# Optimization experiments

Hardware: AMD Instinct MI355X
Metric: run time of the kernel (lower is better)

Reference implementation:

```python
import jax, jax.numpy as jnp
import numpy as np

THETA = 10000.0

def _rope_cache(seq_len, d_k, dtype=jnp.float32):
    # theta_k = theta ** (-(2i/d_k)), angles[n, i] = n * theta_k[i]
    inv_freq = THETA ** (-(jnp.arange(0, d_k, 2, dtype=jnp.float32) / d_k))
    pos = jnp.arange(seq_len, dtype=jnp.float32)
    ang = pos[:, None] * inv_freq[None, :]          # [S, d_k/2]
    cos = jnp.repeat(jnp.cos(ang), 2, axis=-1)      # [S, d_k]
    sin = jnp.repeat(jnp.sin(ang), 2, axis=-1)
    return cos.astype(dtype), sin.astype(dtype)

def _apply_rope(x, cos, sin):
    # x: [..., S, d_k]; rotate even/odd pairs: rot[2i] = -x[2i+1], rot[2i+1] = x[2i]
    x2 = x.reshape(x.shape[:-1] + (x.shape[-1] // 2, 2))
    rot = jnp.stack([-x2[..., 1], x2[..., 0]], axis=-1).reshape(x.shape)
    return x * cos + rot * sin

def setup_inputs() -> dict:
    key = jax.random.key(0)
    ks = jax.random.split(key, 5)
    B, S, D = 2, 2048, 1024
    H, DK = 16, 64
    scale = (2.0 / (D + DK)) ** 0.5
    x = jax.random.normal(ks[0], (B, S, D), dtype=jnp.float32)
    Wq = jax.random.normal(ks[1], (H, D, DK), dtype=jnp.float32) * scale
    Wk = jax.random.normal(ks[2], (H, D, DK), dtype=jnp.float32) * scale
    Wv = jax.random.normal(ks[3], (H, D, DK), dtype=jnp.float32) * scale
    Wo = jax.random.normal(ks[4], (D, D), dtype=jnp.float32) * (2.0 / (2 * D)) ** 0.5
    return {"x": x, "Wq": Wq, "Wk": Wk, "Wv": Wv, "Wo": Wo}

def reference(x, Wq, Wk, Wv, Wo):
    B, S, D = x.shape
    H, _, DK = Wq.shape
    cos, sin = _rope_cache(S, DK, x.dtype)          # [S, DK]
    q = jnp.einsum('bsd,hdk->bhsk', x, Wq)
    k = jnp.einsum('bsd,hdk->bhsk', x, Wk)
    v = jnp.einsum('bsd,hdk->bhsk', x, Wv)
    q = _apply_rope(q, cos, sin)
    k = _apply_rope(k, cos, sin)
    scores = jnp.einsum('bhqk,bhsk->bhqs', q, k) / jnp.sqrt(jnp.asarray(DK, x.dtype))
    causal = jnp.tril(jnp.ones((S, S), dtype=bool))
    scores = jnp.where(causal, scores, -jnp.inf)
    attn = jax.nn.softmax(scores, axis=-1)
    out = jnp.einsum('bhqs,bhsk->bhqk', attn, v)    # [B,H,S,DK]
    out = out.transpose(0, 2, 1, 3).reshape(B, S, H * DK)  # concat heads
    return jnp.einsum('bsd,do->bso', out, Wo)
```

## Files before the change

### kernel.cpp

```cpp
#include <hip/hip_runtime.h>
#include <math.h>

typedef __attribute__((ext_vector_type(8))) short bf16x8;
typedef __attribute__((ext_vector_type(4))) float f32x4;
typedef __attribute__((ext_vector_type(16))) float f32x16;
typedef __attribute__((ext_vector_type(4))) unsigned int uint32x4;
typedef __attribute__((ext_vector_type(2))) unsigned int uint32x2;
typedef unsigned short ushort_t;
typedef unsigned int uint_t;

typedef const void __attribute__((address_space(1)))* gas_ptr;
typedef void __attribute__((address_space(3)))* las_ptr;

namespace {

constexpr int S_  = 2048;
constexpr int D_  = 1024;
constexpr float CSC = 0.18033688011f;

__device__ inline ushort_t f2bf(float f) {
    uint_t u = __builtin_bit_cast(uint_t, f);
    u += 0x7FFFu + ((u >> 16) & 1u);
    return (ushort_t)(u >> 16);
}
__device__ inline uint_t cvtpk(float lo, float hi) {
    uint_t r;
    asm("v_cvt_pk_bf16_f32 %0, %1, %2" : "=v"(r) : "v"(lo), "v"(hi));
    return r;
}
__device__ inline void plswap(uint_t& d, uint_t& s) {
    uint32x2 r = __builtin_amdgcn_permlane32_swap(d, s, false, false);
    d = r[0];
    s = r[1];
}
__device__ inline float xhalf_sum(float x) {
    uint_t d = __builtin_bit_cast(uint_t, x), s = d;
    plswap(d, s);
    return __builtin_bit_cast(float, d) + __builtin_bit_cast(float, s);
}

__device__ inline void tconv_body(const float* __restrict__ src,
                                  ushort_t* __restrict__ dst,
                                  int R, int C, int r0, int c0, int tid)
{
    __shared__ float Tl[64][65];
    #pragma unroll
    for (int l = 0; l < 4; ++l) {
        int i = tid + l * 256;
        int row = i >> 4, col = (i & 15) * 4;
        float4 v = *(const float4*)(src + (size_t)(r0 + row) * C + c0 + col);
        Tl[row][col] = v.x; Tl[row][col + 1] = v.y;
        Tl[row][col + 2] = v.z; Tl[row][col + 3] = v.w;
    }
    __syncthreads();
    #pragma unroll
    for (int l = 0; l < 4; ++l) {
        int i = tid + l * 256;
        int cc = i >> 4, rr = (i & 15) * 4;
        uint_t lo = (uint_t)f2bf(Tl[rr][cc])     | ((uint_t)f2bf(Tl[rr + 1][cc]) << 16);
        uint_t hi = (uint_t)f2bf(Tl[rr + 2][cc]) | ((uint_t)f2bf(Tl[rr + 3][cc]) << 16);
        *(uint2*)(dst + (size_t)(c0 + cc) * R + r0 + rr) = make_uint2(lo, hi);
    }
}

__global__ __launch_bounds__(256)
void prep_kernel(const float* __restrict__ x,  const float* __restrict__ Wq,
                 const float* __restrict__ Wk, const float* __restrict__ Wv,
                 const float* __restrict__ Wo,
                 ushort_t* __restrict__ xb, ushort_t* __restrict__ Wt,
                 ushort_t* __restrict__ Wot, float* __restrict__ tbl)
{
    const int b = blockIdx.x, tid = threadIdx.x;
    if (b < 2048) {
        int i = b * 256 + tid;
        float4 a = ((const float4*)x)[i * 2];
        float4 c = ((const float4*)x)[i * 2 + 1];
        uint_t u0 = (uint_t)f2bf(a.x) | ((uint_t)f2bf(a.y) << 16);
        uint_t u1 = (uint_t)f2bf(a.z) | ((uint_t)f2bf(a.w) << 16);
        uint_t u2 = (uint_t)f2bf(c.x) | ((uint_t)f2bf(c.y) << 16);
        uint_t u3 = (uint_t)f2bf(c.z) | ((uint_t)f2bf(c.w) << 16);
        ((uint4*)xb)[i] = make_uint4(u0, u1, u2, u3);
    } else if (b < 2304) {
        int i = (b - 2048) * 256 + tid;
        int s = i >> 5, p = i & 31;
        float inv = powf(10000.0f, -(float)p * (1.0f / 32.0f));
        float sn, cs;
        sincosf((float)s * inv, &sn, &cs);
        ((float2*)tbl)[i] = make_float2(cs, sn);
    } else if (b < 3072) {
        int lin = b - 2304;
        int z = lin >> 4, rx = lin & 15;
        const float* src = (z < 16 ? Wq : z < 32 ? Wk : Wv) + (size_t)(z & 15) * 65536;
        tconv_body(src, Wt + (size_t)z * 65536, 1024, 64, rx * 64, 0, tid);
    } else {
        int lin = b - 3072;
        tconv_body(Wo, Wot, 1024, 1024, (lin & 15) * 64, (lin >> 4) * 64, tid);
    }
}

__global__ __launch_bounds__(256)
void gemm_kernel(const ushort_t* __restrict__ A, const ushort_t* __restrict__ Bt,
                 ushort_t* __restrict__ Qo, ushort_t* __restrict__ Ko,
                 ushort_t* __restrict__ Vto,
                 const float* __restrict__ tbl, int K)
{
    __shared__ char smem[49152];

    const int tid  = threadIdx.x;
    const int w    = tid >> 6, lane = tid & 63;
    const int lq   = lane & 15, lk = lane >> 4;
    const int wr   = w >> 1, wc = w & 1;
    const int m0   = blockIdx.x * 128;
    const int n0   = blockIdx.y * 128;

    f32x4 acc[4][4] = {};

    const int c0s  = tid, c1s = 256 + tid;
    const int row0 = c0s >> 2, cc0 = (c0s & 3) * 8;
    const int row1 = c1s >> 2, cc1 = (c1s & 3) * 8;
    const ushort_t* gA0 = A  + (size_t)(m0 + row0) * K + cc0;
    const ushort_t* gA1 = A  + (size_t)(m0 + row1) * K + cc1;
    const ushort_t* gB0 = Bt + (size_t)(n0 + row0) * K + cc0;
    const ushort_t* gB1 = Bt + (size_t)(n0 + row1) * K + cc1;
    const int lds0 = c0s * 16;
    const int lds1 = c1s * 16;

    auto stage = [&](int buf, int k0) {
        char* As = smem + buf * 16384;
        char* Bs = As + 8192;
        __builtin_amdgcn_global_load_lds((gas_ptr)(gA0 + k0), (las_ptr)(As + lds0), 16, 0, 0);
        __builtin_amdgcn_global_load_lds((gas_ptr)(gA1 + k0), (las_ptr)(As + lds1), 16, 0, 0);
        __builtin_amdgcn_global_load_lds((gas_ptr)(gB0 + k0), (las_ptr)(Bs + lds0), 16, 0, 0);
        __builtin_amdgcn_global_load_lds((gas_ptr)(gB1 + k0), (las_ptr)(Bs + lds1), 16, 0, 0);
    };

    stage(0, 0);

    const int NT = K >> 5;
    int cur = 0, nx = 1;
    for (int t = 0; t < NT; ++t) {
        if (t < NT - 1) {
            stage(nx, (t + 1) << 5);
            asm volatile("s_waitcnt vmcnt(4)" ::: "memory");
        } else {
            asm volatile("s_waitcnt vmcnt(0)" ::: "memory");
        }
        __builtin_amdgcn_s_barrier();
        asm volatile("" ::: "memory");

        const char* As = smem + cur * 16384;
        const char* Bs = As + 8192;
        bf16x8 a[4], b[4];
        #pragma unroll
        for (int m = 0; m < 4; ++m)
            a[m] = *(const bf16x8*)(As + (wr * 64 + m * 16 + lq) * 64 + lk * 16);
        #pragma unroll
        for (int n = 0; n < 4; ++n)
            b[n] = *(const bf16x8*)(Bs + (wc * 64 + n * 16 + lq) * 64 + lk * 16);
        #pragma unroll
        for (int m = 0; m < 4; ++m)
            #pragma unroll
            for (int n = 0; n < 4; ++n)
                acc[m][n] = __builtin_amdgcn_mfma_f32_16x16x32_bf16(a[m], b[n], acc[m][n], 0, 0, 0);

        asm volatile("" ::: "memory");

        cur = (cur == 2) ? 0 : cur + 1;
        nx  = (nx  == 2) ? 0 : nx  + 1;
    }

    __syncthreads();

    const int sel = n0 >> 10;
    ushort_t* EP = (ushort_t*)smem;
    const int h0 = (n0 & 1023) >> 6;
    if (sel < 2) {
        const float sc = (sel == 0) ? CSC : 1.0f;
        #pragma unroll
        for (int m = 0; m < 4; ++m) {
            #pragma unroll
            for (int r = 0; r < 4; ++r) {
                int lrow = wr * 64 + m * 16 + lk * 4 + r;
                int sG = (m0 + lrow) & 2047;
                #pragma unroll
                for (int n = 0; n < 4; ++n) {
                    int lcol = wc * 64 + n * 16 + lq;
                    int dk = lcol & 63;
                    float v = acc[m][n][r] * sc;
                    float2 cs = *(const float2*)(tbl + ((size_t)sG * 32 + (dk >> 1)) * 2);
                    float sp = __shfl_xor(v, 1);
                    float rv = (dk & 1) ? (v * cs.x + sp * cs.y)
                                        : (v * cs.x - sp * cs.y);
                    EP[lrow * 136 + lcol] = f2bf(rv);
                }
            }
        }
        __syncthreads();
        ushort_t* dst = (sel == 0) ? Qo : Ko;
        #pragma unroll
        for (int it = 0; it < 8; ++it) {
            int idx = it * 256 + tid;
            int row = idx >> 4, c16 = idx & 15;
            uint4 v = *(const uint4*)(EP + row * 136 + c16 * 8);
            int mg = m0 + row;
            int b_ = mg >> 11, s = mg & 2047;
            int h = h0 + (c16 >> 3);
            int dk0 = (c16 & 7) * 8;
            *(uint4*)(dst + (((size_t)b_ * 16 + h) * 2048 + s) * 64 + dk0) = v;
        }
    } else {
        #pragma unroll
        for (int m = 0; m < 4; ++m) {
            #pragma unroll
            for (int r = 0; r < 4; ++r) {
                int lrow = wr * 64 + m * 16 + lk * 4 + r;
                #pragma unroll
                for (int n = 0; n < 4; ++n) {
                    int lcol = wc * 64 + n * 16 + lq;
                    EP[lcol * 136 + lrow] = f2bf(acc[m][n][r]);
                }
            }
        }
        __syncthreads();
        #pragma unroll
        for (int it = 0; it < 8; ++it) {
            int idx = it * 256 + tid;
            int col = idx >> 4, c16 = idx & 15;
            uint4 v = *(const uint4*)(EP + col * 136 + c16 * 8);
            int h = h0 + (col >> 6);
            int dk = col & 63;
            int sb = m0 + c16 * 8;
            int b_ = sb >> 11, s = sb & 2047;
            *(uint4*)(Vto + (((size_t)b_ * 16 + h) * 64 + dk) * 2048 + s) = v;
        }
    }
}

__global__ __launch_bounds__(256)
void gemm2_kernel(const ushort_t* __restrict__ A, const ushort_t* __restrict__ Bt,
                  float* __restrict__ Co, int K)
{
    __shared__ char smem[36864];

    const int tid = threadIdx.x;
    const int w = tid >> 6, lane = tid & 63;
    const int lq = lane & 15, lk = lane >> 4;
    const int wr = w >> 1, wc = w & 1;
    const int m0 = blockIdx.x * 64;
    const int n0 = blockIdx.y * 128;

    f32x4 acc[2][4] = {};

    const int rowA = tid >> 2, cA = (tid & 3) * 8;
    const ushort_t* gA = A + (size_t)(m0 + rowA) * K + cA;
    const int sB0 = tid, sB1 = 256 + tid;
    const int rB0 = sB0 >> 2, cB0 = (sB0 & 3) * 8;
    const int rB1 = sB1 >> 2, cB1 = (sB1 & 3) * 8;
    const ushort_t* gB0 = Bt + (size_t)(n0 + rB0) * K + cB0;
    const ushort_t* gB1 = Bt + (size_t)(n0 + rB1) * K + cB1;

    auto stage = [&](int buf, int k0) {
        char* base = smem + buf * 12288;
        __builtin_amdgcn_global_load_lds((gas_ptr)(gA + k0),  (las_ptr)(base + tid * 16), 16, 0, 0);
        __builtin_amdgcn_global_load_lds((gas_ptr)(gB0 + k0), (las_ptr)(base + 4096 + sB0 * 16), 16, 0, 0);
        __builtin_amdgcn_global_load_lds((gas_ptr)(gB1 + k0), (las_ptr)(base + 4096 + sB1 * 16), 16, 0, 0);
    };

    stage(0, 0);

    const int NT = K >> 5;
    int cur = 0, nx = 1;
    for (int t = 0; t < NT; ++t) {
        if (t < NT - 1) {
            stage(nx, (t + 1) << 5);
            asm volatile("s_waitcnt vmcnt(3)" ::: "memory");
        } else {
            asm volatile("s_waitcnt vmcnt(0)" ::: "memory");
        }
        __builtin_amdgcn_s_barrier();
        asm volatile("" ::: "memory");

        const char* As = smem + cur * 12288;
        const char* Bs = As + 4096;
        bf16x8 a[2], b[4];
        #pragma unroll
        for (int m = 0; m < 2; ++m)
            a[m] = *(const bf16x8*)(As + (wr * 32 + m * 16 + lq) * 64 + lk * 16);
        #pragma unroll
        for (int n = 0; n < 4; ++n)
            b[n] = *(const bf16x8*)(Bs + (wc * 64 + n * 16 + lq) * 64 + lk * 16);
        #pragma unroll
        for (int m = 0; m < 2; ++m)
            #pragma unroll
            for (int n = 0; n < 4; ++n)
                acc[m][n] = __builtin_amdgcn_mfma_f32_16x16x32_bf16(a[m], b[n], acc[m][n], 0, 0, 0);

        asm volatile("" ::: "memory");

        cur = (cur == 2) ? 0 : cur + 1;
        nx  = (nx  == 2) ? 0 : nx  + 1;
    }

    float* EPf = (float*)smem;
    #pragma unroll
    for (int c = 0; c < 2; ++c) {
        __syncthreads();
        if (wr == c) {
            #pragma unroll
            for (int m = 0; m < 2; ++m)
                #pragma unroll
                for (int r = 0; r < 4; ++r) {
                    int lrow = m * 16 + lk * 4 + r;
                    #pragma unroll
                    for (int n = 0; n < 4; ++n) {
                        int lcol = wc * 64 + n * 16 + lq;
                        EPf[lrow * 132 + lcol] = acc[m][n][r];
                    }
                }
        }
        __syncthreads();
        #pragma unroll
        for (int it = 0; it < 4; ++it) {
            int idx = it * 256 + tid;
            int rl = idx >> 5, c32 = idx & 31;
            float4 v = *(const float4*)(EPf + rl * 132 + c32 * 4);
            *(float4*)(Co + (size_t)(m0 + c * 32 + rl) * D_ + n0 + c32 * 4) = v;
        }
    }
}

__global__ __launch_bounds__(512)
void attn_kernel(const ushort_t* __restrict__ Q, const ushort_t* __restrict__ Kg,
                 const ushort_t* __restrict__ Vt, ushort_t* __restrict__ O)
{
    __shared__ ushort_t Ks[2][128 * 64];
    __shared__ ushort_t Vs[2][64 * 128];

    const int bid = blockIdx.x;
    const int p  = 31 - (bid >> 5);
    const int bh = bid & 31;

    const int tid = threadIdx.x;
    const int w = tid >> 6, lane = tid & 63;
    const int wq = w & 1, st = w >> 1;
    const int lq = lane & 31, hi = lane >> 5;
    const size_t bhBase = (size_t)bh * S_ * 64;

    const int nt   = (p >> 1) + 1;
    const int qrel = ((p & 1) << 1) + wq;

    bf16x8 qf[4];
    {
        const ushort_t* qp = Q + bhBase + (size_t)(p * 64 + wq * 32 + lq) * 64 + hi * 8;
        qf[0] = *(const bf16x8*)(qp);
        qf[1] = *(const bf16x8*)(qp + 16);
        qf[2] = *(const bf16x8*)(qp + 32);
        qf[3] = *(const bf16x8*)(qp + 48);
    }

    const int slot0 = tid, slot1 = 512 + tid;
    const int rK0 = slot0 >> 3, rK1 = slot1 >> 3;
    const int rV0 = slot0 >> 4, rV1 = slot1 >> 4;
    const ushort_t* gk0 = Kg + bhBase + (size_t)rK0 * 64 + ((slot0 & 7) ^ (rK0 & 7)) * 8;
    const ushort_t* gk1 = Kg + bhBase + (size_t)rK1 * 64 + ((slot1 & 7) ^ (rK1 & 7)) * 8;
    const ushort_t* gv0 = Vt + bhBase + (size_t)rV0 * 2048 + ((slot0 & 15) ^ (rV0 & 7)) * 8;
    const ushort_t* gv1 = Vt + bhBase + (size_t)rV1 * 2048 + ((slot1 & 15) ^ (rV1 & 7)) * 8;

    auto stage = [&](int buf, int t) {
        const size_t ko = (size_t)t * 128 * 64;
        const size_t vo = (size_t)t * 128;
        __builtin_amdgcn_global_load_lds((gas_ptr)(gk0 + ko), (las_ptr)((char*)Ks[buf] + slot0 * 16), 16, 0, 0);
        __builtin_amdgcn_global_load_lds((gas_ptr)(gk1 + ko), (las_ptr)((char*)Ks[buf] + slot1 * 16), 16, 0, 0);
        __builtin_amdgcn_global_load_lds((gas_ptr)(gv0 + vo), (las_ptr)((char*)Vs[buf] + slot0 * 16), 16, 0, 0);
        __builtin_amdgcn_global_load_lds((gas_ptr)(gv1 + vo), (las_ptr)((char*)Vs[buf] + slot1 * 16), 16, 0, 0);
    };

    float l = 0.0f;
    f32x16 oacc[2] = {};

    const int krow = st * 32 + lq;

    stage(0, 0);

    for (int t = 0; t < nt; ++t) {
        const int cur = t & 1;
        if (t < nt - 1) {
            stage(cur ^ 1, t + 1);
            asm volatile("s_waitcnt vmcnt(4)" ::: "memory");
        } else {
            asm volatile("s_waitcnt vmcnt(0)" ::: "memory");
        }
        __builtin_amdgcn_s_barrier();
        asm volatile("" ::: "memory");

        const bool last = (t == nt - 1);
        if (!(last && st > qrel)) {
            f32x16 sacc = {};
            #pragma unroll
            for (int c = 0; c < 4; ++c) {
                int koff = krow * 128 + ((c * 32 + hi * 16) ^ ((krow & 7) << 4));
                bf16x8 kf = *(const bf16x8*)((const char*)Ks[cur] + koff);
                sacc = __builtin_amdgcn_mfma_f32_32x32x16_bf16(kf, qf[c], sacc, 0, 0, 0);
            }

            if (last && st == qrel) {
                #pragma unroll
                for (int idx = 0; idx < 16; ++idx) {
                    int kvl = (idx & 3) + 8 * (idx >> 2) + 4 * hi;
                    if (kvl > lq) sacc[idx] = -1e30f;
                }
            }

            float pv[16];
            #pragma unroll
            for (int idx = 0; idx < 16; ++idx) {
                float v = exp2f(sacc[idx] - 32.0f);
                pv[idx] = v;
                l += v;
            }

            #pragma unroll
            for (int c2 = 0; c2 < 2; ++c2) {
                uint_t w0 = cvtpk(pv[8 * c2 + 0], pv[8 * c2 + 1]);
                uint_t w1 = cvtpk(pv[8 * c2 + 2], pv[8 * c2 + 3]);
                uint_t w2 = cvtpk(pv[8 * c2 + 4], pv[8 * c2 + 5]);
                uint_t w3 = cvtpk(pv[8 * c2 + 6], pv[8 * c2 + 7]);
                plswap(w0, w2);
                plswap(w1, w3);
                uint32x4 pw; pw[0] = w0; pw[1] = w1; pw[2] = w2; pw[3] = w3;
                bf16x8 pb = __builtin_bit_cast(bf16x8, pw);
                #pragma unroll
                for (int d2 = 0; d2 < 2; ++d2) {
                    int vrow = d2 * 32 + lq;
                    int vslot = (st * 4 + c2 * 2 + hi) ^ (vrow & 7);
                    bf16x8 vf = *(const bf16x8*)((const char*)Vs[cur] + vrow * 256 + vslot * 16);
                    oacc[d2] = __builtin_amdgcn_mfma_f32_32x32x16_bf16(vf, pb, oacc[d2], 0, 0, 0);
                }
            }
        }
        asm volatile("" ::: "memory");
        __builtin_amdgcn_s_barrier();
        asm volatile("" ::: "memory");
    }

    l = xhalf_sum(l);

    __syncthreads();

    float* ksf = (float*)Ks;
    float* vsf = (float*)Vs;
    const int rowi = wq * 64 + lane;
    vsf[st * 128 + rowi] = l;
    if (st == 3) {
        #pragma unroll
        for (int j = 0; j < 8; ++j) {
            f32x4 v4;
            v4[0] = oacc[j >> 2][(j & 3) * 4 + 0];
            v4[1] = oacc[j >> 2][(j & 3) * 4 + 1];
            v4[2] = oacc[j >> 2][(j & 3) * 4 + 2];
            v4[3] = oacc[j >> 2][(j & 3) * 4 + 3];
            *(f32x4*)(ksf + rowi * 32 + ((j ^ (rowi & 7)) * 4)) = v4;
        }
    }
    __syncthreads();
    if (st == 2) {
        #pragma unroll
        for (int j = 0; j < 8; ++j) {
            int soff = rowi * 32 + ((j ^ (rowi & 7)) * 4);
            f32x4 v4 = *(const f32x4*)(ksf + soff);
            v4[0] += oacc[j >> 2][(j & 3) * 4 + 0];
            v4[1] += oacc[j >> 2][(j & 3) * 4 + 1];
            v4[2] += oacc[j >> 2][(j & 3) * 4 + 2];
            v4[3] += oacc[j >> 2][(j & 3) * 4 + 3];
            *(f32x4*)(ksf + soff) = v4;
        }
    }
    __syncthreads();
    if (st == 1) {
        #pragma unroll
        for (int j = 0; j < 8; ++j) {
            int soff = rowi * 32 + ((j ^ (rowi & 7)) * 4);
            f32x4 v4 = *(const f32x4*)(ksf + soff);
            v4[0] += oacc[j >> 2][(j & 3) * 4 + 0];
            v4[1] += oacc[j >> 2][(j & 3) * 4 + 1];
            v4[2] += oacc[j >> 2][(j & 3) * 4 + 2];
            v4[3] += oacc[j >> 2][(j & 3) * 4 + 3];
            *(f32x4*)(ksf + soff) = v4;
        }
    }
    __syncthreads();
    if (st == 0) {
        float lt = vsf[rowi] + vsf[128 + rowi] + vsf[256 + rowi] + vsf[384 + rowi];
        float inv = 1.0f / lt;
        const int b_ = bh >> 4, h = bh & 15;
        const int s = p * 64 + wq * 32 + lq;
        ushort_t* ob = O + ((size_t)b_ * 2048 + s) * 1024 + h * 64;
        #pragma unroll
        for (int j = 0; j < 8; ++j) {
            int soff = rowi * 32 + ((j ^ (rowi & 7)) * 4);
            f32x4 v4 = *(const f32x4*)(ksf + soff);
            int d2 = j >> 2, base = (j & 3) * 4;
            float q0 = (oacc[d2][base + 0] + v4[0]) * inv;
            float q1 = (oacc[d2][base + 1] + v4[1]) * inv;
            float q2 = (oacc[d2][base + 2] + v4[2]) * inv;
            float q3 = (oacc[d2][base + 3] + v4[3]) * inv;
            uint2 pkv;
            pkv.x = cvtpk(q0, q1);
            pkv.y = cvtpk(q2, q3);
            *(uint2*)(ob + d2 * 32 + 8 * (j & 3) + 4 * hi) = pkv;
        }
    }
}

}

extern "C" void kernel_launch(void* const* d_in, const int* in_sizes, int n_in,
                              void* d_out, int out_size, void* d_ws, size_t ws_size,
                              hipStream_t stream)
{
    const float* x  = (const float*)d_in[0];
    const float* Wq = (const float*)d_in[1];
    const float* Wk = (const float*)d_in[2];
    const float* Wv = (const float*)d_in[3];
    const float* Wo = (const float*)d_in[4];

    ushort_t* xb  = (ushort_t*)d_ws;
    ushort_t* Wt  = xb  + 4194304;
    ushort_t* Wot = Wt  + 3145728;
    ushort_t* Qb  = Wot + 1048576;
    ushort_t* Kb  = Qb  + 4194304;
    ushort_t* Vtb = Kb  + 4194304;
    ushort_t* Ob  = Vtb + 4194304;
    float*    tbl = (float*)(Ob + 4194304);

    prep_kernel<<<3328, 256, 0, stream>>>(x, Wq, Wk, Wv, Wo, xb, Wt, Wot, tbl);

    gemm_kernel<<<dim3(32, 24), 256, 0, stream>>>(xb, Wt, Qb, Kb, Vtb, tbl, 1024);

    attn_kernel<<<1024, 512, 0, stream>>>(Qb, Kb, Vtb, Ob);

    gemm2_kernel<<<dim3(64, 8), 256, 0, stream>>>(Ob, Wot, (float*)d_out, 1024);
}
```

Baseline: 103.7 us.

## Widen attention query tile to 128 rows per block with two key splits

Each attention block now covers 128 query rows: four query warps times two key-split groups, instead of 64 rows with four key splits. Each staged K/V tile is therefore reused by twice as many queries, halving global K/V traffic and the block count. The cross-warp reduction at the end shrinks from a four-way to a two-way combine. Block order is changed to mix long and short causal rows. In exchange each warp handles two 32-key chunks per tile, and there are fewer blocks to balance the causal work across CUs.

```diff
diff --git a/kernel.cpp b/kernel.cpp
--- a/kernel.cpp
+++ b/kernel.cpp
@@ -337,21 +337,23 @@
     __shared__ ushort_t Vs[2][64 * 128];
 
     const int bid = blockIdx.x;
-    const int p  = 31 - (bid >> 5);
-    const int bh = bid & 31;
+    const int cch = bid >> 8;
+    const int jj  = bid & 255;
+    const int pg  = jj >> 5;
+    const int bh  = jj & 31;
+    const int P   = cch ? pg : 15 - pg;
 
     const int tid = threadIdx.x;
     const int w = tid >> 6, lane = tid & 63;
-    const int wq = w & 1, st = w >> 1;
+    const int wq = w & 3, st = w >> 2;
     const int lq = lane & 31, hi = lane >> 5;
     const size_t bhBase = (size_t)bh * S_ * 64;
 
-    const int nt   = (p >> 1) + 1;
-    const int qrel = ((p & 1) << 1) + wq;
+    const int nt = P + 1;
 
     bf16x8 qf[4];
     {
-        const ushort_t* qp = Q + bhBase + (size_t)(p * 64 + wq * 32 + lq) * 64 + hi * 8;
+        const ushort_t* qp = Q + bhBase + (size_t)(P * 128 + wq * 32 + lq) * 64 + hi * 8;
         qf[0] = *(const bf16x8*)(qp);
         qf[1] = *(const bf16x8*)(qp + 16);
         qf[2] = *(const bf16x8*)(qp + 32);
@@ -378,8 +380,6 @@
     float l = 0.0f;
     f32x16 oacc[2] = {};
 
-    const int krow = st * 32 + lq;
-
     stage(0, 0);
 
     for (int t = 0; t < nt; ++t) {
@@ -394,16 +394,25 @@
         asm volatile("" ::: "memory");
 
         const bool last = (t == nt - 1);
-        if (!(last && st > qrel)) {
+        #pragma unroll
+        for (int ch = 0; ch < 2; ++ch) {
+            bool tri = false;
+            if (last) {
+                int kb = st * 2 + ch;
+                if (kb > wq) continue;
+                tri = (kb == wq);
+            }
+
+            const int krow = st * 64 + ch * 32 + lq;
             f32x16 sacc = {};
             #pragma unroll
-            for (int c = 0; c < 4; ++c) {
-                int koff = krow * 128 + ((c * 32 + hi * 16) ^ ((krow & 7) << 4));
+            for (int cc = 0; cc < 4; ++cc) {
+                int koff = krow * 128 + ((cc * 32 + hi * 16) ^ ((krow & 7) << 4));
                 bf16x8 kf = *(const bf16x8*)((const char*)Ks[cur] + koff);
-                sacc = __builtin_amdgcn_mfma_f32_32x32x16_bf16(kf, qf[c], sacc, 0, 0, 0);
-            }
-
-            if (last && st == qrel) {
+                sacc = __builtin_amdgcn_mfma_f32_32x32x16_bf16(kf, qf[cc], sacc, 0, 0, 0);
+            }
+
+            if (tri) {
                 #pragma unroll
                 for (int idx = 0; idx < 16; ++idx) {
                     int kvl = (idx & 3) + 8 * (idx >> 2) + 4 * hi;
@@ -432,7 +441,7 @@
                 #pragma unroll
                 for (int d2 = 0; d2 < 2; ++d2) {
                     int vrow = d2 * 32 + lq;
-                    int vslot = (st * 4 + c2 * 2 + hi) ^ (vrow & 7);
+                    int vslot = (st * 8 + ch * 4 + c2 * 2 + hi) ^ (vrow & 7);
                     bf16x8 vf = *(const bf16x8*)((const char*)Vs[cur] + vrow * 256 + vslot * 16);
                     oacc[d2] = __builtin_amdgcn_mfma_f32_32x32x16_bf16(vf, pb, oacc[d2], 0, 0, 0);
                 }
@@ -450,56 +459,30 @@
     float* ksf = (float*)Ks;
     float* vsf = (float*)Vs;
     const int rowi = wq * 64 + lane;
-    vsf[st * 128 + rowi] = l;
-    if (st == 3) {
-        #pragma unroll
-        for (int j = 0; j < 8; ++j) {
+    vsf[st * 256 + rowi] = l;
+    if (st == 1) {
+        #pragma unroll
+        for (int j2 = 0; j2 < 8; ++j2) {
             f32x4 v4;
-            v4[0] = oacc[j >> 2][(j & 3) * 4 + 0];
-            v4[1] = oacc[j >> 2][(j & 3) * 4 + 1];
-            v4[2] = oacc[j >> 2][(j & 3) * 4 + 2];
-            v4[3] = oacc[j >> 2][(j & 3) * 4 + 3];
-            *(f32x4*)(ksf + rowi * 32 + ((j ^ (rowi & 7)) * 4)) = v4;
-        }
-    }
-    __syncthreads();
-    if (st == 2) {
-        #pragma unroll
-        for (int j = 0; j < 8; ++j) {
-            int soff = rowi * 32 + ((j ^ (rowi & 7)) * 4);
-            f32x4 v4 = *(const f32x4*)(ksf + soff);
-            v4[0] += oacc[j >> 2][(j & 3) * 4 + 0];
-            v4[1] += oacc[j >> 2][(j & 3) * 4 + 1];
-            v4[2] += oacc[j >> 2][(j & 3) * 4 + 2];
-            v4[3] += oacc[j >> 2][(j & 3) * 4 + 3];
-            *(f32x4*)(ksf + soff) = v4;
-        }
-    }
-    __syncthreads();
-    if (st == 1) {
-        #pragma unroll
-        for (int j = 0; j < 8; ++j) {
-            int soff = rowi * 32 + ((j ^ (rowi & 7)) * 4);
-            f32x4 v4 = *(const f32x4*)(ksf + soff);
-            v4[0] += oacc[j >> 2][(j & 3) * 4 + 0];
-            v4[1] += oacc[j >> 2][(j & 3) * 4 + 1];
-            v4[2] += oacc[j >> 2][(j & 3) * 4 + 2];
-            v4[3] += oacc[j >> 2][(j & 3) * 4 + 3];
-            *(f32x4*)(ksf + soff) = v4;
+            v4[0] = oacc[j2 >> 2][(j2 & 3) * 4 + 0];
+            v4[1] = oacc[j2 >> 2][(j2 & 3) * 4 + 1];
+            v4[2] = oacc[j2 >> 2][(j2 & 3) * 4 + 2];
+            v4[3] = oacc[j2 >> 2][(j2 & 3) * 4 + 3];
+            *(f32x4*)(ksf + rowi * 32 + ((j2 ^ (rowi & 7)) * 4)) = v4;
         }
     }
     __syncthreads();
     if (st == 0) {
-        float lt = vsf[rowi] + vsf[128 + rowi] + vsf[256 + rowi] + vsf[384 + rowi];
+        float lt = vsf[rowi] + vsf[256 + rowi];
         float inv = 1.0f / lt;
         const int b_ = bh >> 4, h = bh & 15;
-        const int s = p * 64 + wq * 32 + lq;
+        const int s = P * 128 + wq * 32 + lq;
         ushort_t* ob = O + ((size_t)b_ * 2048 + s) * 1024 + h * 64;
         #pragma unroll
-        for (int j = 0; j < 8; ++j) {
-            int soff = rowi * 32 + ((j ^ (rowi & 7)) * 4);
+        for (int j2 = 0; j2 < 8; ++j2) {
+            int soff = rowi * 32 + ((j2 ^ (rowi & 7)) * 4);
             f32x4 v4 = *(const f32x4*)(ksf + soff);
-            int d2 = j >> 2, base = (j & 3) * 4;
+            int d2 = j2 >> 2, base = (j2 & 3) * 4;
             float q0 = (oacc[d2][base + 0] + v4[0]) * inv;
             float q1 = (oacc[d2][base + 1] + v4[1]) * inv;
             float q2 = (oacc[d2][base + 2] + v4[2]) * inv;
@@ -507,7 +490,7 @@
             uint2 pkv;
             pkv.x = cvtpk(q0, q1);
             pkv.y = cvtpk(q2, q3);
-            *(uint2*)(ob + d2 * 32 + 8 * (j & 3) + 4 * hi) = pkv;
+            *(uint2*)(ob + d2 * 32 + 8 * (j2 & 3) + 4 * hi) = pkv;
         }
     }
 }
@@ -537,7 +520,7 @@
 
     gemm_kernel<<<dim3(32, 24), 256, 0, stream>>>(xb, Wt, Qb, Kb, Vtb, tbl, 1024);
 
-    attn_kernel<<<1024, 512, 0, stream>>>(Qb, Kb, Vtb, Ob);
+    attn_kernel<<<512, 512, 0, stream>>>(Qb, Kb, Vtb, Ob);
 
     gemm2_kernel<<<dim3(64, 8), 256, 0, stream>>>(Ob, Wot, (float*)d_out, 1024);
 }
```

New measurement: 103.6 us. No clear change (-0.1%).
